# Performance work log

Hardware: AMD Instinct MI355X
Metric: run time of the kernel (lower is better)

Reference implementation:

```python
import jax, jax.numpy as jnp
import numpy as np

B, T, IN, H, L = 512, 1024, 128, 64, 2  # batch, seq_len, input_size, hidden_size, num_layers
G = 4 * H  # i,f,g,o gates (PyTorch order)


def setup_inputs() -> dict:
    key = jax.random.key(0)
    ks = jax.random.split(key, 7)
    s = 1.0 / np.sqrt(H)  # PyTorch LSTM init bound
    x = jax.random.normal(ks[0], (B, T, IN), dtype=jnp.float32)
    # [num_layers, num_directions(fwd,bwd), 4H, in] -- layer1 in = 2H = IN = 128
    w_ih = jax.random.uniform(ks[1], (L, 2, G, IN), jnp.float32, -s, s)
    w_hh = jax.random.uniform(ks[2], (L, 2, G, H), jnp.float32, -s, s)
    b_ih = jax.random.uniform(ks[3], (L, 2, G), jnp.float32, -s, s)
    b_hh = jax.random.uniform(ks[4], (L, 2, G), jnp.float32, -s, s)
    sf = 1.0 / np.sqrt(2 * H)
    fc_w = jax.random.uniform(ks[5], (1, 2 * H), jnp.float32, -sf, sf)
    fc_b = jax.random.uniform(ks[6], (1,), jnp.float32, -sf, sf)
    return {"x": x, "w_ih": w_ih, "w_hh": w_hh, "b_ih": b_ih, "b_hh": b_hh,
            "fc_w": fc_w, "fc_b": fc_b}


def _lstm_dir(x, w_ih, w_hh, b, reverse):
    # x: [B,T,F]; precompute the input projection as one big GEMM
    gx = jnp.einsum('btf,gf->btg', x, w_ih) + b  # [B,T,4H]
    h0 = jnp.zeros((x.shape[0], H), x.dtype)
    c0 = jnp.zeros((x.shape[0], H), x.dtype)

    def step(carry, g_t):
        h, c = carry
        g = g_t + h @ w_hh.T  # [B,4H]
        i, f, gg, o = jnp.split(g, 4, axis=-1)
        i = jax.nn.sigmoid(i)
        f = jax.nn.sigmoid(f)
        gg = jnp.tanh(gg)
        o = jax.nn.sigmoid(o)
        c = f * c + i * gg
        h = o * jnp.tanh(c)
        return (h, c), h

    _, hs = jax.lax.scan(step, (h0, c0), jnp.swapaxes(gx, 0, 1), reverse=reverse)
    return jnp.swapaxes(hs, 0, 1)  # [B,T,H]; for reverse, hs[t] = state after scanning T-1..t (matches PyTorch)


def reference(x, w_ih, w_hh, b_ih, b_hh, fc_w, fc_b):
    h = x
    for l in range(L):
        b = b_ih[l] + b_hh[l]  # [2,4H]
        fwd = _lstm_dir(h, w_ih[l, 0], w_hh[l, 0], b[0], False)
        bwd = _lstm_dir(h, w_ih[l, 1], w_hh[l, 1], b[1], True)
        h = jnp.concatenate([fwd, bwd], axis=-1)  # [B,T,2H]
    last = h[:, -1, :]  # [B,2H]
    return last @ fc_w.T + fc_b  # [B,1]
```

## Files before the change

### kernel.cpp

```cpp
#include <hip/hip_runtime.h>
#include <hip/hip_bf16.h>

#define TT 1024
#define BB 512

typedef _Float16 half_t;
typedef __attribute__((ext_vector_type(8))) _Float16 v8h;
typedef __attribute__((ext_vector_type(4))) float v4f;

__device__ __forceinline__ float sigf(float x) {
    return __builtin_amdgcn_rcpf(1.0f + __expf(-x));
}
__device__ __forceinline__ float tanhfast(float x) {
    return fmaf(2.0f, __builtin_amdgcn_rcpf(1.0f + __expf(-2.0f * x)), -1.0f);
}

__device__ __forceinline__ void barrier_lds_only() {
    asm volatile("s_waitcnt lgkmcnt(0)\n\ts_barrier" ::: "memory");
}

template<int R, bool IN_F32, bool W16, bool WRITE_SEQ, bool WRITE_LAST>
__global__ __launch_bounds__(256, 1)
void lstm_scan(const void* __restrict__ in_v, const half_t* __restrict__ w16,
               const float* __restrict__ w_ih, const float* __restrict__ w_hh,
               const float* __restrict__ b_ih, const float* __restrict__ b_hh,
               int layer, int use_grid_dir,
               half_t* __restrict__ out_seq, float* __restrict__ out_last)
{
    const int dir = use_grid_dir ? blockIdx.y : 0;
    const int wrow = layer * 2 + dir;
    const int col_off = dir * 64;
    const int b0 = blockIdx.x * R;
    const int wv = threadIdx.x >> 6;
    const int l  = threadIdx.x & 63;
    const int q  = l >> 4;
    const int n16 = l & 15;
    const int j = wv * 16 + n16;
    const int rowc = ((n16 >> 2) < R) ? (n16 >> 2) : (R - 1);

    __shared__ __align__(16) half_t hs[2][16][72];
    {
        v8h z;
        #pragma unroll
        for (int e = 0; e < 8; ++e) z[e] = (half_t)0.f;
        ((v8h*)hs)[threadIdx.x] = z;
        if (threadIdx.x < 32) ((v8h*)hs)[256 + threadIdx.x] = z;
    }

    v8h wb[4][6];
    v4f bseed[4];
    #pragma unroll
    for (int gt = 0; gt < 4; ++gt) {
        const int grow = wrow * 256 + gt * 64 + j;
        if constexpr (W16) {
            const half_t* p = w16 + (size_t)grow * 192 + q * 8;
            #pragma unroll
            for (int kt = 0; kt < 6; ++kt) wb[gt][kt] = *(const v8h*)(p + kt * 32);
        } else {
            const float* pih = w_ih + (size_t)grow * 128 + q * 8;
            #pragma unroll
            for (int kt = 0; kt < 4; ++kt) {
                const float4 a = *(const float4*)(pih + kt * 32);
                const float4 b = *(const float4*)(pih + kt * 32 + 4);
                v8h f;
                f[0] = (half_t)a.x; f[1] = (half_t)a.y; f[2] = (half_t)a.z; f[3] = (half_t)a.w;
                f[4] = (half_t)b.x; f[5] = (half_t)b.y; f[6] = (half_t)b.z; f[7] = (half_t)b.w;
                wb[gt][kt] = f;
            }
            const float* phh = w_hh + (size_t)grow * 64 + q * 8;
            #pragma unroll
            for (int kt = 0; kt < 2; ++kt) {
                const float4 a = *(const float4*)(phh + kt * 32);
                const float4 b = *(const float4*)(phh + kt * 32 + 4);
                v8h f;
                f[0] = (half_t)a.x; f[1] = (half_t)a.y; f[2] = (half_t)a.z; f[3] = (half_t)a.w;
                f[4] = (half_t)b.x; f[5] = (half_t)b.y; f[6] = (half_t)b.z; f[7] = (half_t)b.w;
                wb[gt][4 + kt] = f;
            }
        }
        const float bs = b_ih[grow] + b_hh[grow];
        bseed[gt] = (v4f){bs, bs, bs, bs};
    }

    const long t0 = dir ? (TT - 1) : 0;
    const long xstep = dir ? -128 : 128;

    const float*  xp32 = nullptr;
    const half_t* xp16 = nullptr;
    if constexpr (IN_F32) xp32 = (const float*)in_v + ((size_t)(b0 + rowc) * TT + t0) * 128 + q * 8;
    else                  xp16 = (const half_t*)in_v + ((size_t)(b0 + rowc) * TT + t0) * 128 + q * 8;

    half_t* op = nullptr;
    if constexpr (WRITE_SEQ) {
        const int qr = (q < R) ? q : (R - 1);
        op = out_seq + ((size_t)(b0 + qr) * TT + t0) * 128 + col_off + j;
    }

    auto load_x = [&](v8h* dst) {
        if constexpr (IN_F32) {
            #pragma unroll
            for (int kt = 0; kt < 4; ++kt) {
                const float4 a = *(const float4*)(xp32 + kt * 32);
                const float4 b = *(const float4*)(xp32 + kt * 32 + 4);
                v8h f;
                f[0] = (half_t)a.x; f[1] = (half_t)a.y; f[2] = (half_t)a.z; f[3] = (half_t)a.w;
                f[4] = (half_t)b.x; f[5] = (half_t)b.y; f[6] = (half_t)b.z; f[7] = (half_t)b.w;
                dst[kt] = f;
            }
        } else {
            #pragma unroll
            for (int kt = 0; kt < 4; ++kt) dst[kt] = *(const v8h*)(xp16 + kt * 32);
        }
    };
    auto adv_x = [&]() { if constexpr (IN_F32) xp32 += xstep; else xp16 += xstep; };

    float c = 0.f, hcur = 0.f;

    auto gxc = [&](const v8h (&xf)[4], v4f (&g)[4]) {
        #pragma unroll
        for (int gt = 0; gt < 4; ++gt) {
            v4f a = __builtin_amdgcn_mfma_f32_16x16x32_f16(xf[0], wb[gt][0], bseed[gt], 0, 0, 0);
            a = __builtin_amdgcn_mfma_f32_16x16x32_f16(xf[1], wb[gt][1], a, 0, 0, 0);
            a = __builtin_amdgcn_mfma_f32_16x16x32_f16(xf[2], wb[gt][2], a, 0, 0, 0);
            a = __builtin_amdgcn_mfma_f32_16x16x32_f16(xf[3], wb[gt][3], a, 0, 0, 0);
            g[gt] = a;
        }
    };

    auto stepf = [&](const v4f (&gcur)[4], const v8h (&xn)[4], v4f (&gnext)[4], int pb) {
        const v8h hf0 = *(const v8h*)&hs[pb][n16][q * 8];
        const v8h hf1 = *(const v8h*)&hs[pb][n16][32 + q * 8];
        v4f acc[4];
        #pragma unroll
        for (int gt = 0; gt < 4; ++gt)
            acc[gt] = __builtin_amdgcn_mfma_f32_16x16x32_f16(hf0, wb[gt][4], gcur[gt], 0, 0, 0);
        #pragma unroll
        for (int gt = 0; gt < 4; ++gt)
            acc[gt] = __builtin_amdgcn_mfma_f32_16x16x32_f16(hf1, wb[gt][5], acc[gt], 0, 0, 0);
        __builtin_amdgcn_sched_barrier(0);
        gxc(xn, gnext);
        const float iv = sigf(acc[0][0]);
        const float fv = sigf(acc[1][0]);
        const float gv = tanhfast(acc[2][0]);
        const float ov = sigf(acc[3][0]);
        c = fv * c + iv * gv;
        const float h = ov * tanhfast(c);
        if (q < R) {
            const half_t h16 = (half_t)h;
            hs[pb ^ 1][4 * q][j] = h16;
            if constexpr (WRITE_SEQ) { *op = h16; op += xstep; }
            hcur = h;
        }
    };

    v8h x0[4], x1[4], x2[4], x3[4];
    v4f ga[4], gb[4];
    load_x(x0); adv_x();
    load_x(x1); adv_x();
    load_x(x2); adv_x();
    gxc(x0, ga);
    barrier_lds_only();

    for (int tt = 0; tt < TT; tt += 4) {
        if (tt + 3 < TT) { load_x(x3); adv_x(); }
        stepf(ga, x1, gb, 0); barrier_lds_only();
        if (tt + 4 < TT) { load_x(x0); adv_x(); }
        stepf(gb, x2, ga, 1); barrier_lds_only();
        if (tt + 5 < TT) { load_x(x1); adv_x(); }
        stepf(ga, x3, gb, 0); barrier_lds_only();
        if (tt + 6 < TT) { load_x(x2); adv_x(); }
        stepf(gb, x0, ga, 1); barrier_lds_only();
    }

    if constexpr (WRITE_LAST) {
        if (q < R) out_last[(size_t)(b0 + q) * 64 + j] = hcur;
    }
}

__global__ __launch_bounds__(256)
void cvt_w(const float* __restrict__ w_ih, const float* __restrict__ w_hh,
           half_t* __restrict__ w16)
{
    const int id = blockIdx.x * 256 + threadIdx.x;
    const int row = id / 192, k = id % 192;
    const float v = (k < 128) ? w_ih[row * 128 + k] : w_hh[row * 64 + (k - 128)];
    w16[id] = (half_t)v;
}

__global__ __launch_bounds__(256)
void cvt_x(const float* __restrict__ in, half_t* __restrict__ out)
{
    const size_t i = ((size_t)blockIdx.x * 256 + threadIdx.x) * 8;
    const float4 a = *(const float4*)(in + i);
    const float4 b = *(const float4*)(in + i + 4);
    v8h f;
    f[0] = (half_t)a.x; f[1] = (half_t)a.y; f[2] = (half_t)a.z; f[3] = (half_t)a.w;
    f[4] = (half_t)b.x; f[5] = (half_t)b.y; f[6] = (half_t)b.z; f[7] = (half_t)b.w;
    *(v8h*)(out + i) = f;
}

__global__ __launch_bounds__(256)
void l2bwd_fc(const half_t* __restrict__ in, const float* __restrict__ w_ih,
              const float* __restrict__ b_ih, const float* __restrict__ b_hh,
              const float* __restrict__ hlast, const float* __restrict__ fc_w,
              const float* __restrict__ fc_b, float* __restrict__ out)
{
    const int b = blockIdx.x;
    const int g = threadIdx.x;
    __shared__ float gpre[256];
    __shared__ float hb[64];

    float acc = b_ih[3 * 256 + g] + b_hh[3 * 256 + g];
    const float* wp = w_ih + ((size_t)(3 * 256 + g)) * 128;
    const half_t* xp = in + ((size_t)b * TT + (TT - 1)) * 128;
    #pragma unroll
    for (int k = 0; k < 128; k += 8) {
        const float4 w0 = *(const float4*)(wp + k);
        const float4 w1 = *(const float4*)(wp + k + 4);
        const v8h xv = *(const v8h*)(xp + k);
        acc = fmaf(w0.x, (float)xv[0], acc); acc = fmaf(w0.y, (float)xv[1], acc);
        acc = fmaf(w0.z, (float)xv[2], acc); acc = fmaf(w0.w, (float)xv[3], acc);
        acc = fmaf(w1.x, (float)xv[4], acc); acc = fmaf(w1.y, (float)xv[5], acc);
        acc = fmaf(w1.z, (float)xv[6], acc); acc = fmaf(w1.w, (float)xv[7], acc);
    }
    gpre[g] = acc;
    __syncthreads();

    if (g < 64) {
        const float i  = sigf(gpre[g]);
        const float gg = tanhfast(gpre[128 + g]);
        const float o  = sigf(gpre[192 + g]);
        hb[g] = o * tanhfast(i * gg);
    }
    __syncthreads();

    if (g < 64) {
        float p = fc_w[g] * hlast[(size_t)b * 64 + g] + fc_w[64 + g] * hb[g];
        #pragma unroll
        for (int off = 32; off > 0; off >>= 1) p += __shfl_down(p, off);
        if (g == 0) out[b] = p + fc_b[0];
    }
}

extern "C" void kernel_launch(void* const* d_in, const int* in_sizes, int n_in,
                              void* d_out, int out_size, void* d_ws, size_t ws_size,
                              hipStream_t stream)
{
    const float* x    = (const float*)d_in[0];
    const float* w_ih = (const float*)d_in[1];
    const float* w_hh = (const float*)d_in[2];
    const float* b_ih = (const float*)d_in[3];
    const float* b_hh = (const float*)d_in[4];
    const float* fc_w = (const float*)d_in[5];
    const float* fc_b = (const float*)d_in[6];
    float* out = (float*)d_out;

    const size_t seq_b   = (size_t)BB * TT * 128 * sizeof(half_t);
    const size_t w16_b   = (size_t)1024 * 192 * sizeof(half_t);
    const size_t hlast_b = (size_t)BB * 64 * sizeof(float);

    if (ws_size >= w16_b + hlast_b + 2 * seq_b) {
        half_t* w16   = (half_t*)d_ws;
        float*  hlast = (float*)((char*)d_ws + w16_b);
        half_t* x16   = (half_t*)((char*)d_ws + w16_b + hlast_b);
        half_t* out1  = (half_t*)((char*)d_ws + w16_b + hlast_b + seq_b);

        cvt_w<<<768, 256, 0, stream>>>(w_ih, w_hh, w16);
        cvt_x<<<(BB * TT * 128 / 8) / 256, 256, 0, stream>>>(x, x16);
        lstm_scan<4, false, true, true, false><<<dim3(BB / 4, 2), 256, 0, stream>>>(
            x16, w16, w_ih, w_hh, b_ih, b_hh, 0, 1, out1, nullptr);
        lstm_scan<4, false, true, false, true><<<dim3(BB / 4, 1), 256, 0, stream>>>(
            out1, w16, w_ih, w_hh, b_ih, b_hh, 1, 0, nullptr, hlast);
        l2bwd_fc<<<BB, 256, 0, stream>>>(out1, w_ih, b_ih, b_hh, hlast, fc_w, fc_b, out);
    } else if (ws_size >= 2 * seq_b + hlast_b) {
        half_t* x16   = (half_t*)d_ws;
        half_t* out1  = (half_t*)((char*)d_ws + seq_b);
        float*  hlast = (float*)((char*)d_ws + 2 * seq_b);

        cvt_x<<<(BB * TT * 128 / 8) / 256, 256, 0, stream>>>(x, x16);
        lstm_scan<4, false, false, true, false><<<dim3(BB / 4, 2), 256, 0, stream>>>(
            x16, nullptr, w_ih, w_hh, b_ih, b_hh, 0, 1, out1, nullptr);
        lstm_scan<4, false, false, false, true><<<dim3(BB / 4, 1), 256, 0, stream>>>(
            out1, nullptr, w_ih, w_hh, b_ih, b_hh, 1, 0, nullptr, hlast);
        l2bwd_fc<<<BB, 256, 0, stream>>>(out1, w_ih, b_ih, b_hh, hlast, fc_w, fc_b, out);
    } else {
        half_t* out1  = (half_t*)d_ws;
        float*  hlast = (float*)((char*)d_ws + seq_b);

        lstm_scan<4, true, false, true, false><<<dim3(BB / 4, 2), 256, 0, stream>>>(
            x, nullptr, w_ih, w_hh, b_ih, b_hh, 0, 1, out1, nullptr);
        lstm_scan<4, false, false, false, true><<<dim3(BB / 4, 1), 256, 0, stream>>>(
            out1, nullptr, w_ih, w_hh, b_ih, b_hh, 1, 0, nullptr, hlast);
        l2bwd_fc<<<BB, 256, 0, stream>>>(out1, w_ih, b_ih, b_hh, hlast, fc_w, fc_b, out);
    }
}
```

Before: 1.221 ms.

## Split LSTM scan into producer waves for input projection and consumer waves for recurrence

```diff
diff --git a/kernel.cpp b/kernel.cpp
--- a/kernel.cpp
+++ b/kernel.cpp
@@ -20,7 +20,7 @@
 }
 
 template<int R, bool IN_F32, bool W16, bool WRITE_SEQ, bool WRITE_LAST>
-__global__ __launch_bounds__(256, 1)
+__global__ __launch_bounds__(512, 2)
 void lstm_scan(const void* __restrict__ in_v, const half_t* __restrict__ w16,
                const float* __restrict__ w_ih, const float* __restrict__ w_hh,
                const float* __restrict__ b_ih, const float* __restrict__ b_hh,
@@ -31,55 +31,75 @@
     const int wrow = layer * 2 + dir;
     const int col_off = dir * 64;
     const int b0 = blockIdx.x * R;
-    const int wv = threadIdx.x >> 6;
-    const int l  = threadIdx.x & 63;
+    const int tid = threadIdx.x;
+    const int wid = tid >> 6;
+    const bool prod = wid >= 4;
+    const int wv = wid & 3;
+    const int l  = tid & 63;
     const int q  = l >> 4;
     const int n16 = l & 15;
     const int j = wv * 16 + n16;
     const int rowc = ((n16 >> 2) < R) ? (n16 >> 2) : (R - 1);
 
     __shared__ __align__(16) half_t hs[2][16][72];
+    __shared__ __align__(16) float  gxr[4][4][64][4];
+
     {
-        v8h z;
-        #pragma unroll
-        for (int e = 0; e < 8; ++e) z[e] = (half_t)0.f;
-        ((v8h*)hs)[threadIdx.x] = z;
-        if (threadIdx.x < 32) ((v8h*)hs)[256 + threadIdx.x] = z;
-    }
-
-    v8h wb[4][6];
+        if (tid < 288) {
+            v8h z;
+            #pragma unroll
+            for (int e = 0; e < 8; ++e) z[e] = (half_t)0.f;
+            ((v8h*)hs)[tid] = z;
+        }
+    }
+
+    v8h wbx[4][4];
     v4f bseed[4];
-    #pragma unroll
-    for (int gt = 0; gt < 4; ++gt) {
-        const int grow = wrow * 256 + gt * 64 + j;
-        if constexpr (W16) {
-            const half_t* p = w16 + (size_t)grow * 192 + q * 8;
-            #pragma unroll
-            for (int kt = 0; kt < 6; ++kt) wb[gt][kt] = *(const v8h*)(p + kt * 32);
-        } else {
-            const float* pih = w_ih + (size_t)grow * 128 + q * 8;
-            #pragma unroll
-            for (int kt = 0; kt < 4; ++kt) {
-                const float4 a = *(const float4*)(pih + kt * 32);
-                const float4 b = *(const float4*)(pih + kt * 32 + 4);
-                v8h f;
-                f[0] = (half_t)a.x; f[1] = (half_t)a.y; f[2] = (half_t)a.z; f[3] = (half_t)a.w;
-                f[4] = (half_t)b.x; f[5] = (half_t)b.y; f[6] = (half_t)b.z; f[7] = (half_t)b.w;
-                wb[gt][kt] = f;
+    v8h wbh[4][2];
+    if (prod) {
+        #pragma unroll
+        for (int gt = 0; gt < 4; ++gt) {
+            const int grow = wrow * 256 + gt * 64 + j;
+            if constexpr (W16) {
+                const half_t* p = w16 + (size_t)grow * 192 + q * 8;
+                #pragma unroll
+                for (int kt = 0; kt < 4; ++kt) wbx[gt][kt] = *(const v8h*)(p + kt * 32);
+            } else {
+                const float* pih = w_ih + (size_t)grow * 128 + q * 8;
+                #pragma unroll
+                for (int kt = 0; kt < 4; ++kt) {
+                    const float4 a = *(const float4*)(pih + kt * 32);
+                    const float4 b = *(const float4*)(pih + kt * 32 + 4);
+                    v8h f;
+                    f[0] = (half_t)a.x; f[1] = (half_t)a.y; f[2] = (half_t)a.z; f[3] = (half_t)a.w;
+                    f[4] = (half_t)b.x; f[5] = (half_t)b.y; f[6] = (half_t)b.z; f[7] = (half_t)b.w;
+                    wbx[gt][kt] = f;
+                }
             }
-            const float* phh = w_hh + (size_t)grow * 64 + q * 8;
-            #pragma unroll
-            for (int kt = 0; kt < 2; ++kt) {
-                const float4 a = *(const float4*)(phh + kt * 32);
-                const float4 b = *(const float4*)(phh + kt * 32 + 4);
-                v8h f;
-                f[0] = (half_t)a.x; f[1] = (half_t)a.y; f[2] = (half_t)a.z; f[3] = (half_t)a.w;
-                f[4] = (half_t)b.x; f[5] = (half_t)b.y; f[6] = (half_t)b.z; f[7] = (half_t)b.w;
-                wb[gt][4 + kt] = f;
+            const float bs = b_ih[grow] + b_hh[grow];
+            bseed[gt] = (v4f){bs, bs, bs, bs};
+        }
+    } else {
+        #pragma unroll
+        for (int gt = 0; gt < 4; ++gt) {
+            const int grow = wrow * 256 + gt * 64 + j;
+            if constexpr (W16) {
+                const half_t* p = w16 + (size_t)grow * 192 + 128 + q * 8;
+                #pragma unroll
+                for (int kt = 0; kt < 2; ++kt) wbh[gt][kt] = *(const v8h*)(p + kt * 32);
+            } else {
+                const float* phh = w_hh + (size_t)grow * 64 + q * 8;
+                #pragma unroll
+                for (int kt = 0; kt < 2; ++kt) {
+                    const float4 a = *(const float4*)(phh + kt * 32);
+                    const float4 b = *(const float4*)(phh + kt * 32 + 4);
+                    v8h f;
+                    f[0] = (half_t)a.x; f[1] = (half_t)a.y; f[2] = (half_t)a.z; f[3] = (half_t)a.w;
+                    f[4] = (half_t)b.x; f[5] = (half_t)b.y; f[6] = (half_t)b.z; f[7] = (half_t)b.w;
+                    wbh[gt][kt] = f;
+                }
             }
         }
-        const float bs = b_ih[grow] + b_hh[grow];
-        bseed[gt] = (v4f){bs, bs, bs, bs};
     }
 
     const long t0 = dir ? (TT - 1) : 0;
@@ -114,37 +134,41 @@
     };
     auto adv_x = [&]() { if constexpr (IN_F32) xp32 += xstep; else xp16 += xstep; };
 
+    auto gxstore = [&](const v8h (&xf)[4], int slot) {
+        v4f g;
+        #pragma unroll
+        for (int gt = 0; gt < 4; ++gt) {
+            v4f a = __builtin_amdgcn_mfma_f32_16x16x32_f16(xf[0], wbx[gt][0], bseed[gt], 0, 0, 0);
+            a = __builtin_amdgcn_mfma_f32_16x16x32_f16(xf[1], wbx[gt][1], a, 0, 0, 0);
+            a = __builtin_amdgcn_mfma_f32_16x16x32_f16(xf[2], wbx[gt][2], a, 0, 0, 0);
+            a = __builtin_amdgcn_mfma_f32_16x16x32_f16(xf[3], wbx[gt][3], a, 0, 0, 0);
+            g[gt] = a[0];
+        }
+        *(v4f*)&gxr[slot][wv][l][0] = g;
+    };
+
     float c = 0.f, hcur = 0.f;
-
-    auto gxc = [&](const v8h (&xf)[4], v4f (&g)[4]) {
-        #pragma unroll
-        for (int gt = 0; gt < 4; ++gt) {
-            v4f a = __builtin_amdgcn_mfma_f32_16x16x32_f16(xf[0], wb[gt][0], bseed[gt], 0, 0, 0);
-            a = __builtin_amdgcn_mfma_f32_16x16x32_f16(xf[1], wb[gt][1], a, 0, 0, 0);
-            a = __builtin_amdgcn_mfma_f32_16x16x32_f16(xf[2], wb[gt][2], a, 0, 0, 0);
-            a = __builtin_amdgcn_mfma_f32_16x16x32_f16(xf[3], wb[gt][3], a, 0, 0, 0);
-            g[gt] = a;
-        }
-    };
-
-    auto stepf = [&](const v4f (&gcur)[4], const v8h (&xn)[4], v4f (&gnext)[4], int pb) {
+    const v4f z4 = {0.f, 0.f, 0.f, 0.f};
+
+    auto cstep = [&](int p, int pb) {
+        __builtin_amdgcn_s_setprio(1);
         const v8h hf0 = *(const v8h*)&hs[pb][n16][q * 8];
         const v8h hf1 = *(const v8h*)&hs[pb][n16][32 + q * 8];
+        const v4f gxl = *(const v4f*)&gxr[p][wv][l][0];
         v4f acc[4];
         #pragma unroll
         for (int gt = 0; gt < 4; ++gt)
-            acc[gt] = __builtin_amdgcn_mfma_f32_16x16x32_f16(hf0, wb[gt][4], gcur[gt], 0, 0, 0);
+            acc[gt] = __builtin_amdgcn_mfma_f32_16x16x32_f16(hf0, wbh[gt][0], z4, 0, 0, 0);
         #pragma unroll
         for (int gt = 0; gt < 4; ++gt)
-            acc[gt] = __builtin_amdgcn_mfma_f32_16x16x32_f16(hf1, wb[gt][5], acc[gt], 0, 0, 0);
-        __builtin_amdgcn_sched_barrier(0);
-        gxc(xn, gnext);
-        const float iv = sigf(acc[0][0]);
-        const float fv = sigf(acc[1][0]);
-        const float gv = tanhfast(acc[2][0]);
-        const float ov = sigf(acc[3][0]);
+            acc[gt] = __builtin_amdgcn_mfma_f32_16x16x32_f16(hf1, wbh[gt][1], acc[gt], 0, 0, 0);
+        const float iv = sigf(acc[0][0] + gxl[0]);
+        const float fv = sigf(acc[1][0] + gxl[1]);
+        const float gv = tanhfast(acc[2][0] + gxl[2]);
+        const float ov = sigf(acc[3][0] + gxl[3]);
         c = fv * c + iv * gv;
         const float h = ov * tanhfast(c);
+        __builtin_amdgcn_s_setprio(0);
         if (q < R) {
             const half_t h16 = (half_t)h;
             hs[pb ^ 1][4 * q][j] = h16;
@@ -154,26 +178,49 @@
     };
 
     v8h x0[4], x1[4], x2[4], x3[4];
-    v4f ga[4], gb[4];
-    load_x(x0); adv_x();
-    load_x(x1); adv_x();
-    load_x(x2); adv_x();
-    gxc(x0, ga);
+    if (prod) {
+        load_x(x0); adv_x();
+        load_x(x1); adv_x();
+        load_x(x2); adv_x();
+        load_x(x3); adv_x();
+        gxstore(x0, 0);
+        gxstore(x1, 1);
+    }
     barrier_lds_only();
 
     for (int tt = 0; tt < TT; tt += 4) {
-        if (tt + 3 < TT) { load_x(x3); adv_x(); }
-        stepf(ga, x1, gb, 0); barrier_lds_only();
-        if (tt + 4 < TT) { load_x(x0); adv_x(); }
-        stepf(gb, x2, ga, 1); barrier_lds_only();
-        if (tt + 5 < TT) { load_x(x1); adv_x(); }
-        stepf(ga, x3, gb, 0); barrier_lds_only();
-        if (tt + 6 < TT) { load_x(x2); adv_x(); }
-        stepf(gb, x0, ga, 1); barrier_lds_only();
+        if (prod) {
+            if (tt + 4 < TT) { load_x(x0); adv_x(); }
+            if (tt + 2 < TT) gxstore(x2, 2);
+        } else {
+            cstep(0, 0);
+        }
+        barrier_lds_only();
+        if (prod) {
+            if (tt + 5 < TT) { load_x(x1); adv_x(); }
+            if (tt + 3 < TT) gxstore(x3, 3);
+        } else {
+            cstep(1, 1);
+        }
+        barrier_lds_only();
+        if (prod) {
+            if (tt + 6 < TT) { load_x(x2); adv_x(); }
+            if (tt + 4 < TT) gxstore(x0, 0);
+        } else {
+            cstep(2, 0);
+        }
+        barrier_lds_only();
+        if (prod) {
+            if (tt + 7 < TT) { load_x(x3); adv_x(); }
+            if (tt + 5 < TT) gxstore(x1, 1);
+        } else {
+            cstep(3, 1);
+        }
+        barrier_lds_only();
     }
 
     if constexpr (WRITE_LAST) {
-        if (q < R) out_last[(size_t)(b0 + q) * 64 + j] = hcur;
+        if (!prod && q < R) out_last[(size_t)(b0 + q) * 64 + j] = hcur;
     }
 }
 
@@ -267,9 +314,9 @@
 
         cvt_w<<<768, 256, 0, stream>>>(w_ih, w_hh, w16);
         cvt_x<<<(BB * TT * 128 / 8) / 256, 256, 0, stream>>>(x, x16);
-        lstm_scan<4, false, true, true, false><<<dim3(BB / 4, 2), 256, 0, stream>>>(
+        lstm_scan<4, false, true, true, false><<<dim3(BB / 4, 2), 512, 0, stream>>>(
             x16, w16, w_ih, w_hh, b_ih, b_hh, 0, 1, out1, nullptr);
-        lstm_scan<4, false, true, false, true><<<dim3(BB / 4, 1), 256, 0, stream>>>(
+        lstm_scan<4, false, true, false, true><<<dim3(BB / 4, 1), 512, 0, stream>>>(
             out1, w16, w_ih, w_hh, b_ih, b_hh, 1, 0, nullptr, hlast);
         l2bwd_fc<<<BB, 256, 0, stream>>>(out1, w_ih, b_ih, b_hh, hlast, fc_w, fc_b, out);
     } else if (ws_size >= 2 * seq_b + hlast_b) {
@@ -278,18 +325,18 @@
         float*  hlast = (float*)((char*)d_ws + 2 * seq_b);
 
         cvt_x<<<(BB * TT * 128 / 8) / 256, 256, 0, stream>>>(x, x16);
-        lstm_scan<4, false, false, true, false><<<dim3(BB / 4, 2), 256, 0, stream>>>(
+        lstm_scan<4, false, false, true, false><<<dim3(BB / 4, 2), 512, 0, stream>>>(
             x16, nullptr, w_ih, w_hh, b_ih, b_hh, 0, 1, out1, nullptr);
-        lstm_scan<4, false, false, false, true><<<dim3(BB / 4, 1), 256, 0, stream>>>(
+        lstm_scan<4, false, false, false, true><<<dim3(BB / 4, 1), 512, 0, stream>>>(
             out1, nullptr, w_ih, w_hh, b_ih, b_hh, 1, 0, nullptr, hlast);
         l2bwd_fc<<<BB, 256, 0, stream>>>(out1, w_ih, b_ih, b_hh, hlast, fc_w, fc_b, out);
     } else {
         half_t* out1  = (half_t*)d_ws;
         float*  hlast = (float*)((char*)d_ws + seq_b);
 
-        lstm_scan<4, true, false, true, false><<<dim3(BB / 4, 2), 256, 0, stream>>>(
+        lstm_scan<4, true, false, true, false><<<dim3(BB / 4, 2), 512, 0, stream>>>(
             x, nullptr, w_ih, w_hh, b_ih, b_hh, 0, 1, out1, nullptr);
-        lstm_scan<4, false, false, false, true><<<dim3(BB / 4, 1), 256, 0, stream>>>(
+        lstm_scan<4, false, false, false, true><<<dim3(BB / 4, 1), 512, 0, stream>>>(
             out1, nullptr, w_ih, w_hh, b_ih, b_hh, 1, 0, nullptr, hlast);
         l2bwd_fc<<<BB, 256, 0, stream>>>(out1, w_ih, b_ih, b_hh, hlast, fc_w, fc_b, out);
     }
```

Result: slower. 1.573 ms (+28.9%).

## Batch input projection over 4 timesteps per MFMA using LDS ring buffer

Applied to the files above, without the earlier changes.

```diff
diff --git a/kernel.cpp b/kernel.cpp
--- a/kernel.cpp
+++ b/kernel.cpp
@@ -31,23 +31,28 @@
     const int wrow = layer * 2 + dir;
     const int col_off = dir * 64;
     const int b0 = blockIdx.x * R;
-    const int wv = threadIdx.x >> 6;
-    const int l  = threadIdx.x & 63;
+    const int tid = threadIdx.x;
+    const int wv = tid >> 6;
+    const int l  = tid & 63;
     const int q  = l >> 4;
     const int n16 = l & 15;
     const int j = wv * 16 + n16;
-    const int rowc = ((n16 >> 2) < R) ? (n16 >> 2) : (R - 1);
+    const int arow = n16 & 3;
+    const int as4  = n16 >> 2;
 
     __shared__ __align__(16) half_t hs[2][16][72];
+    __shared__ __align__(16) float ring[2][4][4][4][16][4];
+
     {
         v8h z;
         #pragma unroll
         for (int e = 0; e < 8; ++e) z[e] = (half_t)0.f;
-        ((v8h*)hs)[threadIdx.x] = z;
-        if (threadIdx.x < 32) ((v8h*)hs)[256 + threadIdx.x] = z;
-    }
-
-    v8h wb[4][6];
+        ((v8h*)hs)[tid] = z;
+        if (tid < 32) ((v8h*)hs)[256 + tid] = z;
+    }
+
+    v8h wbx[4][4];
+    v8h wbh[4][2];
     v4f bseed[4];
     #pragma unroll
     for (int gt = 0; gt < 4; ++gt) {
@@ -55,7 +60,9 @@
         if constexpr (W16) {
             const half_t* p = w16 + (size_t)grow * 192 + q * 8;
             #pragma unroll
-            for (int kt = 0; kt < 6; ++kt) wb[gt][kt] = *(const v8h*)(p + kt * 32);
+            for (int kt = 0; kt < 4; ++kt) wbx[gt][kt] = *(const v8h*)(p + kt * 32);
+            #pragma unroll
+            for (int kt = 0; kt < 2; ++kt) wbh[gt][kt] = *(const v8h*)(p + 128 + kt * 32);
         } else {
             const float* pih = w_ih + (size_t)grow * 128 + q * 8;
             #pragma unroll
@@ -65,7 +72,7 @@
                 v8h f;
                 f[0] = (half_t)a.x; f[1] = (half_t)a.y; f[2] = (half_t)a.z; f[3] = (half_t)a.w;
                 f[4] = (half_t)b.x; f[5] = (half_t)b.y; f[6] = (half_t)b.z; f[7] = (half_t)b.w;
-                wb[gt][kt] = f;
+                wbx[gt][kt] = f;
             }
             const float* phh = w_hh + (size_t)grow * 64 + q * 8;
             #pragma unroll
@@ -75,7 +82,7 @@
                 v8h f;
                 f[0] = (half_t)a.x; f[1] = (half_t)a.y; f[2] = (half_t)a.z; f[3] = (half_t)a.w;
                 f[4] = (half_t)b.x; f[5] = (half_t)b.y; f[6] = (half_t)b.z; f[7] = (half_t)b.w;
-                wb[gt][4 + kt] = f;
+                wbh[gt][kt] = f;
             }
         }
         const float bs = b_ih[grow] + b_hh[grow];
@@ -85,91 +92,96 @@
     const long t0 = dir ? (TT - 1) : 0;
     const long xstep = dir ? -128 : 128;
 
-    const float*  xp32 = nullptr;
-    const half_t* xp16 = nullptr;
-    if constexpr (IN_F32) xp32 = (const float*)in_v + ((size_t)(b0 + rowc) * TT + t0) * 128 + q * 8;
-    else                  xp16 = (const half_t*)in_v + ((size_t)(b0 + rowc) * TT + t0) * 128 + q * 8;
-
     half_t* op = nullptr;
     if constexpr (WRITE_SEQ) {
-        const int qr = (q < R) ? q : (R - 1);
-        op = out_seq + ((size_t)(b0 + qr) * TT + t0) * 128 + col_off + j;
-    }
-
-    auto load_x = [&](v8h* dst) {
+        op = out_seq + ((size_t)(b0 + q) * TT + t0) * 128 + col_off + j;
+    }
+
+    const half_t* gld16 = nullptr;
+    const float*  gld32 = nullptr;
+    auto set_gld = [&](int t4) {
+        int t4c = (t4 > TT - 4) ? (TT - 4) : t4;
+        const int tt = dir ? (TT - 1 - (t4c + as4)) : (t4c + as4);
+        const size_t off = ((size_t)(b0 + arow) * TT + tt) * 128 + q * 8;
+        if constexpr (IN_F32) gld32 = (const float*)in_v + off;
+        else                  gld16 = (const half_t*)in_v + off;
+    };
+    auto ldfrag = [&](int kt) -> v8h {
         if constexpr (IN_F32) {
-            #pragma unroll
-            for (int kt = 0; kt < 4; ++kt) {
-                const float4 a = *(const float4*)(xp32 + kt * 32);
-                const float4 b = *(const float4*)(xp32 + kt * 32 + 4);
-                v8h f;
-                f[0] = (half_t)a.x; f[1] = (half_t)a.y; f[2] = (half_t)a.z; f[3] = (half_t)a.w;
-                f[4] = (half_t)b.x; f[5] = (half_t)b.y; f[6] = (half_t)b.z; f[7] = (half_t)b.w;
-                dst[kt] = f;
-            }
+            const float4 a = *(const float4*)(gld32 + kt * 32);
+            const float4 b = *(const float4*)(gld32 + kt * 32 + 4);
+            v8h f;
+            f[0] = (half_t)a.x; f[1] = (half_t)a.y; f[2] = (half_t)a.z; f[3] = (half_t)a.w;
+            f[4] = (half_t)b.x; f[5] = (half_t)b.y; f[6] = (half_t)b.z; f[7] = (half_t)b.w;
+            return f;
         } else {
-            #pragma unroll
-            for (int kt = 0; kt < 4; ++kt) dst[kt] = *(const v8h*)(xp16 + kt * 32);
+            return *(const v8h*)(gld16 + kt * 32);
         }
     };
-    auto adv_x = [&]() { if constexpr (IN_F32) xp32 += xstep; else xp16 += xstep; };
+
+    auto gx_gate = [&](const v8h (&xf)[4], int gt) -> v4f {
+        v4f a = __builtin_amdgcn_mfma_f32_16x16x32_f16(xf[0], wbx[gt][0], bseed[gt], 0, 0, 0);
+        a = __builtin_amdgcn_mfma_f32_16x16x32_f16(xf[1], wbx[gt][1], a, 0, 0, 0);
+        a = __builtin_amdgcn_mfma_f32_16x16x32_f16(xf[2], wbx[gt][2], a, 0, 0, 0);
+        a = __builtin_amdgcn_mfma_f32_16x16x32_f16(xf[3], wbx[gt][3], a, 0, 0, 0);
+        return a;
+    };
 
     float c = 0.f, hcur = 0.f;
-
-    auto gxc = [&](const v8h (&xf)[4], v4f (&g)[4]) {
+    const v4f z4 = {0.f, 0.f, 0.f, 0.f};
+
+    auto run_group = [&](int bufR, const v8h (&xc)[4], v8h (&xn)[4]) {
+        const int bufW = bufR ^ 1;
+        xn[0] = ldfrag(0); xn[1] = ldfrag(1); xn[2] = ldfrag(2); xn[3] = ldfrag(3);
         #pragma unroll
-        for (int gt = 0; gt < 4; ++gt) {
-            v4f a = __builtin_amdgcn_mfma_f32_16x16x32_f16(xf[0], wb[gt][0], bseed[gt], 0, 0, 0);
-            a = __builtin_amdgcn_mfma_f32_16x16x32_f16(xf[1], wb[gt][1], a, 0, 0, 0);
-            a = __builtin_amdgcn_mfma_f32_16x16x32_f16(xf[2], wb[gt][2], a, 0, 0, 0);
-            a = __builtin_amdgcn_mfma_f32_16x16x32_f16(xf[3], wb[gt][3], a, 0, 0, 0);
-            g[gt] = a;
-        }
-    };
-
-    auto stepf = [&](const v4f (&gcur)[4], const v8h (&xn)[4], v4f (&gnext)[4], int pb) {
-        const v8h hf0 = *(const v8h*)&hs[pb][n16][q * 8];
-        const v8h hf1 = *(const v8h*)&hs[pb][n16][32 + q * 8];
-        v4f acc[4];
-        #pragma unroll
-        for (int gt = 0; gt < 4; ++gt)
-            acc[gt] = __builtin_amdgcn_mfma_f32_16x16x32_f16(hf0, wb[gt][4], gcur[gt], 0, 0, 0);
-        #pragma unroll
-        for (int gt = 0; gt < 4; ++gt)
-            acc[gt] = __builtin_amdgcn_mfma_f32_16x16x32_f16(hf1, wb[gt][5], acc[gt], 0, 0, 0);
-        __builtin_amdgcn_sched_barrier(0);
-        gxc(xn, gnext);
-        const float iv = sigf(acc[0][0]);
-        const float fv = sigf(acc[1][0]);
-        const float gv = tanhfast(acc[2][0]);
-        const float ov = sigf(acc[3][0]);
-        c = fv * c + iv * gv;
-        const float h = ov * tanhfast(c);
-        if (q < R) {
+        for (int s = 0; s < 4; ++s) {
+            const int pb = s & 1;
+            const v8h hf0 = *(const v8h*)&hs[pb][n16][q * 8];
+            const v8h hf1 = *(const v8h*)&hs[pb][n16][32 + q * 8];
+            const float g0 = ring[bufR][wv][s][0][n16][q];
+            const float g1 = ring[bufR][wv][s][1][n16][q];
+            const float g2 = ring[bufR][wv][s][2][n16][q];
+            const float g3 = ring[bufR][wv][s][3][n16][q];
+            const v4f gg = gx_gate(xc, s);
+            v4f acc[4];
+            #pragma unroll
+            for (int gt = 0; gt < 4; ++gt)
+                acc[gt] = __builtin_amdgcn_mfma_f32_16x16x32_f16(hf0, wbh[gt][0], z4, 0, 0, 0);
+            #pragma unroll
+            for (int gt = 0; gt < 4; ++gt)
+                acc[gt] = __builtin_amdgcn_mfma_f32_16x16x32_f16(hf1, wbh[gt][1], acc[gt], 0, 0, 0);
+            const float iv = sigf(acc[0][0] + g0);
+            const float fv = sigf(acc[1][0] + g1);
+            const float gv = tanhfast(acc[2][0] + g2);
+            const float ov = sigf(acc[3][0] + g3);
+            c = fv * c + iv * gv;
+            const float h = ov * tanhfast(c);
+            *(v4f*)&ring[bufW][wv][q][s][n16][0] = gg;
             const half_t h16 = (half_t)h;
             hs[pb ^ 1][4 * q][j] = h16;
             if constexpr (WRITE_SEQ) { *op = h16; op += xstep; }
             hcur = h;
+            barrier_lds_only();
         }
     };
 
-    v8h x0[4], x1[4], x2[4], x3[4];
-    v4f ga[4], gb[4];
-    load_x(x0); adv_x();
-    load_x(x1); adv_x();
-    load_x(x2); adv_x();
-    gxc(x0, ga);
+    v8h xt[4], xA[4], xB[4];
+    set_gld(0);
+    xt[0] = ldfrag(0); xt[1] = ldfrag(1); xt[2] = ldfrag(2); xt[3] = ldfrag(3);
+    set_gld(4);
+    xA[0] = ldfrag(0); xA[1] = ldfrag(1); xA[2] = ldfrag(2); xA[3] = ldfrag(3);
+    #pragma unroll
+    for (int gt = 0; gt < 4; ++gt) {
+        const v4f g0 = gx_gate(xt, gt);
+        *(v4f*)&ring[0][wv][q][gt][n16][0] = g0;
+    }
     barrier_lds_only();
 
-    for (int tt = 0; tt < TT; tt += 4) {
-        if (tt + 3 < TT) { load_x(x3); adv_x(); }
-        stepf(ga, x1, gb, 0); barrier_lds_only();
-        if (tt + 4 < TT) { load_x(x0); adv_x(); }
-        stepf(gb, x2, ga, 1); barrier_lds_only();
-        if (tt + 5 < TT) { load_x(x1); adv_x(); }
-        stepf(ga, x3, gb, 0); barrier_lds_only();
-        if (tt + 6 < TT) { load_x(x2); adv_x(); }
-        stepf(gb, x0, ga, 1); barrier_lds_only();
+    for (int g = 0; g < TT / 4; g += 2) {
+        set_gld(4 * g + 8);
+        run_group(0, xA, xB);
+        set_gld(4 * g + 12);
+        run_group(1, xB, xA);
     }
 
     if constexpr (WRITE_LAST) {
```

New measurement: 1.016 ms. 1.2x faster.
